# Optimization experiments

Hardware: AMD Instinct MI355X
Metric: run time of the kernel (lower is better)

## Reference

```python
import jax, jax.numpy as jnp
import numpy as np

EMBED_DIM = 1024
HEADS = 16
HEAD_DIM = EMBED_DIM // HEADS


def setup_inputs() -> dict:
    key = jax.random.key(0)
    k1, k2, k3, k4 = jax.random.split(key, 4)
    x = jax.random.normal(k1, (4, 2048, EMBED_DIM), dtype=jnp.float32)
    # nn.Linear weights stored as (out, in); apply as x @ W.T
    W_qkv = jax.random.normal(k2, (3 * EMBED_DIM, EMBED_DIM), dtype=jnp.float32) / np.sqrt(EMBED_DIM)
    W_out = jax.random.normal(k3, (EMBED_DIM, EMBED_DIM), dtype=jnp.float32) / np.sqrt(EMBED_DIM)
    b_out = jax.random.normal(k4, (EMBED_DIM,), dtype=jnp.float32) * 0.02
    return {"x": x, "W_qkv": W_qkv, "W_out": W_out, "b_out": b_out}


def reference(x, W_qkv, W_out, b_out):
    B, N, _ = x.shape
    qkv = jnp.einsum('bnd,ed->bne', x, W_qkv)  # (B, N, 3*E)
    q, k, v = jnp.split(qkv, 3, axis=-1)
    # (B, H, N, Dh)
    q = q.reshape(B, N, HEADS, HEAD_DIM).transpose(0, 2, 1, 3)
    k = k.reshape(B, N, HEADS, HEAD_DIM).transpose(0, 2, 1, 3)
    v = v.reshape(B, N, HEADS, HEAD_DIM).transpose(0, 2, 1, 3)
    scale = 1.0 / np.sqrt(HEAD_DIM).astype(np.float32)
    scores = jnp.einsum('bhqd,bhkd->bhqk', q, k) * scale  # (B, H, N, N)
    attn = jax.nn.softmax(scores, axis=-1)
    out = jnp.einsum('bhqk,bhkd->bhqd', attn, v)  # (B, H, N, Dh)
    out = out.transpose(0, 2, 1, 3).reshape(B, N, EMBED_DIM)
    return jnp.einsum('bne,oe->bno', out, W_out) + b_out
```

## Files before the change

kernel.cpp:

```cpp
#include <hip/hip_runtime.h>
#include <hip/hip_bf16.h>
#include <stdint.h>


typedef _Float16 half8 __attribute__((ext_vector_type(8)));
typedef _Float16 half4 __attribute__((ext_vector_type(4)));
typedef __fp16 fp16x2 __attribute__((ext_vector_type(2)));
typedef float floatx4 __attribute__((ext_vector_type(4)));

#define E 1024
#define NH 16
#define DH 64
#define SEQ 2048
#define BATCH 4

__device__ __forceinline__ void gload_lds16(const void* g, void* lds) {
  typedef __attribute__((address_space(1))) void gv;
  typedef __attribute__((address_space(3))) void lv;
  __builtin_amdgcn_global_load_lds((gv*)g, (lv*)lds, 16, 0, 0);
}

__device__ __forceinline__ float fast_exp2(float x) {
#if __has_builtin(__builtin_amdgcn_exp2f)
  return __builtin_amdgcn_exp2f(x);
#else
  return exp2f(x);
#endif
}

__device__ __forceinline__ float max3f(float a, float b, float c) {
  return fmaxf(fmaxf(a, b), c);
}

__global__ __launch_bounds__(256)
void cvt3_f32_f16(const float* __restrict__ a, _Float16* __restrict__ oa, int na,
                  const float* __restrict__ b, _Float16* __restrict__ ob, int nb,
                  const float* __restrict__ c, _Float16* __restrict__ oc, int nc) {
  int i = blockIdx.x * 256 + threadIdx.x;
  const float* in;
  _Float16* out;
  int idx;
  if (i < na) { in = a; out = oa; idx = i; }
  else if (i < na + nb) { in = b; out = ob; idx = i - na; }
  else if (i < na + nb + nc) { in = c; out = oc; idx = i - na - nb; }
  else return;
  const float4* p = (const float4*)in;
  float4 u = p[2 * idx], v = p[2 * idx + 1];
  half8 h;
  h[0] = (_Float16)u.x; h[1] = (_Float16)u.y; h[2] = (_Float16)u.z; h[3] = (_Float16)u.w;
  h[4] = (_Float16)v.x; h[5] = (_Float16)v.y; h[6] = (_Float16)v.z; h[7] = (_Float16)v.w;
  ((half8*)out)[idx] = h;
}

__global__ __launch_bounds__(256)
void gemm_qkv(const _Float16* __restrict__ A, const _Float16* __restrict__ W,
              _Float16* __restrict__ qo, _Float16* __restrict__ ko, _Float16* __restrict__ vt) {
  __shared__ __align__(16) _Float16 As[128 * 64];
  __shared__ __align__(16) _Float16 Bs[128 * 64];
  const int t = threadIdx.x;
  const int w = t >> 6, l = t & 63;
  const int wr = w >> 1, wc = w & 1;
  const int lr = l & 15, hi = l >> 4;
  const int tileRow = blockIdx.y * 128;
  const int tileCol = blockIdx.x * 128;
  const int ldsW = (t & ~63) * 16;
  floatx4 acc[4][4] = {};

  for (int k0 = 0; k0 < 1024; k0 += 64) {
    __syncthreads();
#pragma unroll
    for (int c = 0; c < 4; ++c) {
      int idx = c * 256 + t;
      int row = idx >> 3, g = idx & 7;
      gload_lds16(A + (size_t)(tileRow + row) * 1024 + k0 + g * 8, (char*)As + c * 4096 + ldsW);
      gload_lds16(W + (size_t)(tileCol + row) * 1024 + k0 + g * 8, (char*)Bs + c * 4096 + ldsW);
    }
    __syncthreads();
#pragma unroll
    for (int kk = 0; kk < 2; ++kk) {
      half8 af[4], bf[4];
#pragma unroll
      for (int m = 0; m < 4; ++m)
        af[m] = *(const half8*)(As + (wr * 64 + m * 16 + lr) * 64 + kk * 32 + hi * 8);
#pragma unroll
      for (int n = 0; n < 4; ++n)
        bf[n] = *(const half8*)(Bs + (wc * 64 + n * 16 + lr) * 64 + kk * 32 + hi * 8);
#pragma unroll
      for (int m = 0; m < 4; ++m)
#pragma unroll
        for (int n = 0; n < 4; ++n)
          acc[m][n] = __builtin_amdgcn_mfma_f32_16x16x32_f16(af[m], bf[n], acc[m][n], 0, 0, 0);
    }
  }
  const int sec = tileCol >> 10;
  const int b = tileRow >> 11;
  const int tokBase = (tileRow & 2047) + wr * 64;
  if (sec == 2) {
#pragma unroll
    for (int n = 0; n < 4; ++n) {
      int col = (tileCol & 1023) + wc * 64 + n * 16 + lr;
      int h = col >> 6, d = col & 63;
      _Float16* base = vt + (((size_t)b * NH + h) * DH + d) * SEQ + tokBase;
#pragma unroll
      for (int m = 0; m < 4; ++m) {
        half4 v;
#pragma unroll
        for (int j = 0; j < 4; ++j) v[j] = (_Float16)acc[m][n][j];
        *(half4*)(base + m * 16 + hi * 4) = v;
      }
    }
  } else {
    _Float16* dst = sec == 0 ? qo : ko;
    const float scaleq = sec == 0 ? 0.18033688011112042f : 1.0f;
#pragma unroll
    for (int n = 0; n < 4; ++n) {
      int col = (tileCol & 1023) + wc * 64 + n * 16 + lr;
      int h = col >> 6, d = col & 63;
      _Float16* base = dst + (((size_t)b * NH + h) * SEQ + tokBase) * DH + d;
#pragma unroll
      for (int m = 0; m < 4; ++m)
#pragma unroll
        for (int j = 0; j < 4; ++j)
          base[(size_t)(m * 16 + hi * 4 + j) * DH] = (_Float16)(acc[m][n][j] * scaleq);
    }
  }
}

__global__ __launch_bounds__(256, 3)
void attn(const _Float16* __restrict__ Q, const _Float16* __restrict__ Kg,
          const _Float16* __restrict__ VT, _Float16* __restrict__ O) {
  __shared__ __align__(16) _Float16 Ks[64 * 64];
  __shared__ __align__(16) _Float16 Vs[64 * 64];
  __shared__ __align__(16) _Float16 Ps[4][16 * 64];
  const int bh = blockIdx.y, qt = blockIdx.x;
  const int t = threadIdx.x, w = t >> 6, l = t & 63;
  const int lr = l & 15, hi = l >> 4;
  const int ldsW = (t & ~63) * 16;
  const _Float16* qb = Q + ((size_t)bh * SEQ + qt * 128 + w * 32) * DH;
  half8 qf[2][2];
#pragma unroll
  for (int g = 0; g < 2; ++g) {
    qf[g][0] = *(const half8*)(qb + (g * 16 + lr) * DH + hi * 8);
    qf[g][1] = *(const half8*)(qb + (g * 16 + lr) * DH + 32 + hi * 8);
  }
  floatx4 o0[4] = {}, o1[4] = {};
  float m0 = 0.f, m1 = 0.f, l0 = 0.f, l1 = 0.f;
  const _Float16* kb = Kg + (size_t)bh * SEQ * DH;
  const _Float16* vb = VT + (size_t)bh * DH * SEQ;
  char* pw = (char*)&Ps[w][0];
  const int lrm = lr & 7;
  uint32_t wra[4], rda[2];
#pragma unroll
  for (int n = 0; n < 4; ++n)
    wra[n] = lr * 128 + ((((2 * n + (hi >> 1)) ^ lrm)) << 4) + (hi & 1) * 8;
#pragma unroll
  for (int kk = 0; kk < 2; ++kk)
    rda[kk] = lr * 128 + (((4 * kk + hi) ^ lrm) << 4);

  auto sm = [&](floatx4(&s)[4], float& mr, float& lsum, floatx4(&oa)[4], fp16x2(&pk)[4][2]) {
    float ma = max3f(s[0][0], s[0][1], s[0][2]);
    float mb = max3f(s[0][3], s[1][0], s[1][1]);
    float mc = max3f(s[1][2], s[1][3], s[2][0]);
    float md = max3f(s[2][1], s[2][2], s[2][3]);
    float me = max3f(s[3][0], s[3][1], s[3][2]);
    float mx = max3f(max3f(ma, mb, mc), fmaxf(md, me), s[3][3]);
    mx = fmaxf(mx, __shfl_xor(mx, 16));
    mx = fmaxf(mx, __shfl_xor(mx, 32));
    float rs = 0.f;
    if (__builtin_expect(__any(mx > 10.f), 0)) {
      float dm = fmaxf(mx, 0.f);
      float fac = fast_exp2(-dm);
      mr += dm;
      lsum *= fac;
#pragma unroll
      for (int j = 0; j < 4; ++j) {
        float fj = __shfl(fac, hi * 4 + j);
#pragma unroll
        for (int n = 0; n < 4; ++n) oa[n][j] *= fj;
      }
#pragma unroll
      for (int n = 0; n < 4; ++n) {
        float p0 = fast_exp2(s[n][0] - dm), p1 = fast_exp2(s[n][1] - dm);
        float p2 = fast_exp2(s[n][2] - dm), p3 = fast_exp2(s[n][3] - dm);
        pk[n][0] = __builtin_amdgcn_cvt_pkrtz(p0, p1);
        pk[n][1] = __builtin_amdgcn_cvt_pkrtz(p2, p3);
        rs += p0 + p1 + p2 + p3;
      }
    } else {
#pragma unroll
      for (int n = 0; n < 4; ++n) {
        float p0 = fast_exp2(s[n][0]), p1 = fast_exp2(s[n][1]);
        float p2 = fast_exp2(s[n][2]), p3 = fast_exp2(s[n][3]);
        pk[n][0] = __builtin_amdgcn_cvt_pkrtz(p0, p1);
        pk[n][1] = __builtin_amdgcn_cvt_pkrtz(p2, p3);
        rs += p0 + p1 + p2 + p3;
      }
    }
    lsum += rs;
  };

  auto proute = [&](fp16x2(&pk)[4][2], half8(&pf)[2]) {
#pragma unroll
    for (int n = 0; n < 4; ++n) {
      uint2 v;
      v.x = __builtin_bit_cast(uint32_t, pk[n][0]);
      v.y = __builtin_bit_cast(uint32_t, pk[n][1]);
      *(uint2*)(pw + wra[n]) = v;
    }
    pf[0] = *(const half8*)(pw + rda[0]);
    pf[1] = *(const half8*)(pw + rda[1]);
  };

  for (int kt = 0; kt < SEQ / 64; ++kt) {
    __syncthreads();
#pragma unroll
    for (int c = 0; c < 2; ++c) {
      int idx = c * 256 + t;
      int row = idx >> 3, g = idx & 7, gs = g ^ (row & 7);
      gload_lds16(kb + (size_t)(kt * 64 + row) * DH + gs * 8, (char*)Ks + c * 4096 + ldsW);
      gload_lds16(vb + (size_t)row * SEQ + kt * 64 + gs * 8, (char*)Vs + c * 4096 + ldsW);
    }
    __syncthreads();
    half8 af[8];
#pragma unroll
    for (int kk = 0; kk < 2; ++kk) {
      int gl = kk * 4 + hi;
#pragma unroll
      for (int n = 0; n < 4; ++n) {
        int key = n * 16 + lr;
        af[kk * 4 + n] = *(const half8*)((char*)Ks + key * 128 + ((gl ^ (key & 7)) << 4));
      }
    }
    floatx4 cb0 = {-m0, -m0, -m0, -m0};
    floatx4 s0[4] = {cb0, cb0, cb0, cb0};
    __builtin_amdgcn_s_setprio(1);
#pragma unroll
    for (int kk = 0; kk < 2; ++kk)
#pragma unroll
      for (int n = 0; n < 4; ++n)
        s0[n] = __builtin_amdgcn_mfma_f32_16x16x32_f16(af[kk * 4 + n], qf[0][kk], s0[n], 0, 0, 0);
    __builtin_amdgcn_s_setprio(0);
    fp16x2 pk[4][2];
    half8 pf[2];
    sm(s0, m0, l0, o0, pk);
    proute(pk, pf);
    floatx4 cb1 = {-m1, -m1, -m1, -m1};
    floatx4 s1[4] = {cb1, cb1, cb1, cb1};
    __builtin_amdgcn_s_setprio(1);
#pragma unroll
    for (int kk = 0; kk < 2; ++kk)
#pragma unroll
      for (int n = 0; n < 4; ++n)
        s1[n] = __builtin_amdgcn_mfma_f32_16x16x32_f16(af[kk * 4 + n], qf[1][kk], s1[n], 0, 0, 0);
    __builtin_amdgcn_s_setprio(0);
    half8 vf[8];
#pragma unroll
    for (int kk = 0; kk < 2; ++kk) {
      int gl = kk * 4 + hi;
#pragma unroll
      for (int n = 0; n < 4; ++n) {
        int d = n * 16 + lr;
        vf[kk * 4 + n] = *(const half8*)((char*)Vs + d * 128 + ((gl ^ (d & 7)) << 4));
      }
    }
    __builtin_amdgcn_s_setprio(1);
#pragma unroll
    for (int kk = 0; kk < 2; ++kk)
#pragma unroll
      for (int n = 0; n < 4; ++n)
        o0[n] = __builtin_amdgcn_mfma_f32_16x16x32_f16(pf[kk], vf[kk * 4 + n], o0[n], 0, 0, 0);
    __builtin_amdgcn_s_setprio(0);
    sm(s1, m1, l1, o1, pk);
    proute(pk, pf);
    __builtin_amdgcn_s_setprio(1);
#pragma unroll
    for (int kk = 0; kk < 2; ++kk)
#pragma unroll
      for (int n = 0; n < 4; ++n)
        o1[n] = __builtin_amdgcn_mfma_f32_16x16x32_f16(pf[kk], vf[kk * 4 + n], o1[n], 0, 0, 0);
    __builtin_amdgcn_s_setprio(0);
  }
  l0 += __shfl_xor(l0, 16); l0 += __shfl_xor(l0, 32);
  l1 += __shfl_xor(l1, 16); l1 += __shfl_xor(l1, 32);
  const int b = bh >> 4, h = bh & 15;
#pragma unroll
  for (int g = 0; g < 2; ++g) {
    const floatx4* oa = g == 0 ? o0 : o1;
    float lg = g == 0 ? l0 : l1;
#pragma unroll
    for (int j = 0; j < 4; ++j) {
      float lj = __shfl(lg, hi * 4 + j);
      float inv = 1.f / lj;
      int tok = qt * 128 + w * 32 + g * 16 + hi * 4 + j;
      _Float16* ob = O + ((size_t)b * SEQ + tok) * E + h * DH;
#pragma unroll
      for (int n = 0; n < 4; ++n) ob[n * 16 + lr] = (_Float16)(oa[n][j] * inv);
    }
  }
}

__global__ __launch_bounds__(256)
void gemm_out(const _Float16* __restrict__ A, const _Float16* __restrict__ W,
              const float* __restrict__ bias, float* __restrict__ out) {
  __shared__ __align__(16) _Float16 As[128 * 64];
  __shared__ __align__(16) _Float16 Bs[128 * 64];
  const int t = threadIdx.x;
  const int w = t >> 6, l = t & 63;
  const int wr = w >> 1, wc = w & 1;
  const int lr = l & 15, hi = l >> 4;
  const int tileRow = blockIdx.y * 128;
  const int tileCol = blockIdx.x * 128;
  const int ldsW = (t & ~63) * 16;
  floatx4 acc[4][4] = {};

  for (int k0 = 0; k0 < 1024; k0 += 64) {
    __syncthreads();
#pragma unroll
    for (int c = 0; c < 4; ++c) {
      int idx = c * 256 + t;
      int row = idx >> 3, g = idx & 7;
      gload_lds16(A + (size_t)(tileRow + row) * 1024 + k0 + g * 8, (char*)As + c * 4096 + ldsW);
      gload_lds16(W + (size_t)(tileCol + row) * 1024 + k0 + g * 8, (char*)Bs + c * 4096 + ldsW);
    }
    __syncthreads();
#pragma unroll
    for (int kk = 0; kk < 2; ++kk) {
      half8 af[4], bf[4];
#pragma unroll
      for (int m = 0; m < 4; ++m)
        af[m] = *(const half8*)(As + (wr * 64 + m * 16 + lr) * 64 + kk * 32 + hi * 8);
#pragma unroll
      for (int n = 0; n < 4; ++n)
        bf[n] = *(const half8*)(Bs + (wc * 64 + n * 16 + lr) * 64 + kk * 32 + hi * 8);
#pragma unroll
      for (int m = 0; m < 4; ++m)
#pragma unroll
        for (int n = 0; n < 4; ++n)
          acc[m][n] = __builtin_amdgcn_mfma_f32_16x16x32_f16(af[m], bf[n], acc[m][n], 0, 0, 0);
    }
  }
#pragma unroll
  for (int n = 0; n < 4; ++n) {
    int col = tileCol + wc * 64 + n * 16 + lr;
    float bv = bias[col];
#pragma unroll
    for (int m = 0; m < 4; ++m) {
      int row = tileRow + wr * 64 + m * 16 + hi * 4;
#pragma unroll
      for (int j = 0; j < 4; ++j)
        out[(size_t)(row + j) * E + col] = acc[m][n][j] + bv;
    }
  }
}

extern "C" void kernel_launch(void* const* d_in, const int* in_sizes, int n_in,
                              void* d_out, int out_size, void* d_ws, size_t ws_size,
                              hipStream_t stream) {
  const float* x = (const float*)d_in[0];
  const float* Wqkv = (const float*)d_in[1];
  const float* Wout = (const float*)d_in[2];
  const float* bout = (const float*)d_in[3];
  float* out = (float*)d_out;
  char* ws = (char*)d_ws;
  _Float16* x16 = (_Float16*)(ws);
  _Float16* q16 = (_Float16*)(ws + (16u << 20));
  _Float16* k16 = (_Float16*)(ws + (32u << 20));
  _Float16* vt16 = (_Float16*)(ws + (48u << 20));
  _Float16* wq16 = (_Float16*)(ws + (64u << 20));
  _Float16* wo16 = (_Float16*)(ws + (70u << 20));
  _Float16* ao16 = x16;

  int n8x = in_sizes[0] / 8, n8q = in_sizes[1] / 8, n8o = in_sizes[2] / 8;
  int n8 = n8x + n8q + n8o;
  cvt3_f32_f16<<<(n8 + 255) / 256, 256, 0, stream>>>(x, x16, n8x, Wqkv, wq16, n8q, Wout, wo16, n8o);
  gemm_qkv<<<dim3(24, 64), 256, 0, stream>>>(x16, wq16, q16, k16, vt16);
  attn<<<dim3(16, 64), 256, 0, stream>>>(q16, k16, vt16, ao16);
  gemm_out<<<dim3(8, 64), 256, 0, stream>>>(ao16, wo16, bout, out);
}
```

Before: 228.8 us.

## Prefetch next K/V tile into registers and remap attention blocks across XCDs

Measured after the change: 278.1 us. 1.22x slower.

```diff
diff --git a/kernel.cpp b/kernel.cpp
--- a/kernel.cpp
+++ b/kernel.cpp
@@ -132,10 +132,11 @@
   __shared__ __align__(16) _Float16 Ks[64 * 64];
   __shared__ __align__(16) _Float16 Vs[64 * 64];
   __shared__ __align__(16) _Float16 Ps[4][16 * 64];
-  const int bh = blockIdx.y, qt = blockIdx.x;
+  const int orig = blockIdx.x;
+  const int nid = (orig & 7) * 128 + (orig >> 3);
+  const int qt = nid & 15, bh = nid >> 4;
   const int t = threadIdx.x, w = t >> 6, l = t & 63;
   const int lr = l & 15, hi = l >> 4;
-  const int ldsW = (t & ~63) * 16;
   const _Float16* qb = Q + ((size_t)bh * SEQ + qt * 128 + w * 32) * DH;
   half8 qf[2][2];
 #pragma unroll
@@ -156,6 +157,24 @@
 #pragma unroll
   for (int kk = 0; kk < 2; ++kk)
     rda[kk] = lr * 128 + (((4 * kk + hi) ^ lrm) << 4);
+
+  uint4 kreg[2], vreg[2];
+  auto load_regs = [&](int kt) {
+#pragma unroll
+    for (int c = 0; c < 2; ++c) {
+      int idx = c * 256 + t;
+      int row = idx >> 3, g = idx & 7, gs = g ^ (row & 7);
+      kreg[c] = *(const uint4*)(kb + (size_t)(kt * 64 + row) * DH + gs * 8);
+      vreg[c] = *(const uint4*)(vb + (size_t)row * SEQ + kt * 64 + gs * 8);
+    }
+  };
+  auto write_lds = [&]() {
+#pragma unroll
+    for (int c = 0; c < 2; ++c) {
+      *(uint4*)((char*)Ks + (c * 256 + t) * 16) = kreg[c];
+      *(uint4*)((char*)Vs + (c * 256 + t) * 16) = vreg[c];
+    }
+  };
 
   auto sm = [&](floatx4(&s)[4], float& mr, float& lsum, floatx4(&oa)[4], fp16x2(&pk)[4][2]) {
     float ma = max3f(s[0][0], s[0][1], s[0][2]);
@@ -211,16 +230,13 @@
     pf[1] = *(const half8*)(pw + rda[1]);
   };
 
-  for (int kt = 0; kt < SEQ / 64; ++kt) {
-    __syncthreads();
-#pragma unroll
-    for (int c = 0; c < 2; ++c) {
-      int idx = c * 256 + t;
-      int row = idx >> 3, g = idx & 7, gs = g ^ (row & 7);
-      gload_lds16(kb + (size_t)(kt * 64 + row) * DH + gs * 8, (char*)Ks + c * 4096 + ldsW);
-      gload_lds16(vb + (size_t)row * SEQ + kt * 64 + gs * 8, (char*)Vs + c * 4096 + ldsW);
-    }
-    __syncthreads();
+  load_regs(0);
+  write_lds();
+  __syncthreads();
+  const int NT = SEQ / 64;
+  for (int kt = 0; kt < NT; ++kt) {
+    const bool more = kt + 1 < NT;
+    if (more) load_regs(kt + 1);
     half8 af[8];
 #pragma unroll
     for (int kk = 0; kk < 2; ++kk) {
@@ -279,6 +295,11 @@
       for (int n = 0; n < 4; ++n)
         o1[n] = __builtin_amdgcn_mfma_f32_16x16x32_f16(pf[kk], vf[kk * 4 + n], o1[n], 0, 0, 0);
     __builtin_amdgcn_s_setprio(0);
+    if (more) {
+      __syncthreads();
+      write_lds();
+      __syncthreads();
+    }
   }
   l0 += __shfl_xor(l0, 16); l0 += __shfl_xor(l0, 32);
   l1 += __shfl_xor(l1, 16); l1 += __shfl_xor(l1, 32);
@@ -374,6 +395,6 @@
   int n8 = n8x + n8q + n8o;
   cvt3_f32_f16<<<(n8 + 255) / 256, 256, 0, stream>>>(x, x16, n8x, Wqkv, wq16, n8q, Wout, wo16, n8o);
   gemm_qkv<<<dim3(24, 64), 256, 0, stream>>>(x16, wq16, q16, k16, vt16);
-  attn<<<dim3(16, 64), 256, 0, stream>>>(q16, k16, vt16, ao16);
+  attn<<<dim3(1024), 256, 0, stream>>>(q16, k16, vt16, ao16);
   gemm_out<<<dim3(8, 64), 256, 0, stream>>>(ao16, wo16, bout, out);
 }
```
